# Kernel tuning notes

Hardware: AMD Instinct MI355X
Metric: run time of the kernel (lower is better)

The kernel has to match this reference:

```python
import jax, jax.numpy as jnp
import numpy as np

B = 131072   # batch (tokens)
D = 512      # d_model
P = 10       # n_programs
H = D // 4   # extractor hidden
MAXO = 4     # max operands
MAXR = 3     # max results


def setup_inputs() -> dict:
    key = jax.random.key(0)
    ks = jax.random.split(key, 6)
    hidden = jax.random.normal(ks[0], (B, D), jnp.float32)
    program_ids = jax.random.randint(ks[1], (B,), 0, P)
    Wr = jax.random.normal(ks[2], (D, P), jnp.float32) * (1.0 / np.sqrt(D))
    br = jnp.zeros((P,), jnp.float32)
    # stacked per-program extractor MLPs, output padded to MAXO (extra cols unused)
    W1 = jax.random.normal(ks[3], (P, D, H), jnp.float32) * (1.0 / np.sqrt(D))
    b1 = jnp.zeros((P, H), jnp.float32)
    W2 = jax.random.normal(ks[4], (P, H, MAXO), jnp.float32) * (1.0 / np.sqrt(H))
    b2 = jnp.zeros((P, MAXO), jnp.float32)
    return {"hidden": hidden, "program_ids": program_ids, "Wr": Wr, "br": br,
            "W1": W1, "b1": b1, "W2": W2, "b2": b2}


def _time_decompose(total_minutes):
    days = jnp.floor(total_minutes / 1440.0)
    rem = total_minutes - days * 1440.0
    hours = jnp.floor(rem / 60.0)
    minutes = rem - hours * 60.0
    return hours, minutes, days


def _safe(b):
    # avoid NaN/Inf from zero denominators in Mod/FloorDiv
    return jnp.where(b == 0, 1.0, b)


def _programs():
    # (fn -> tuple of result arrays, n_operands), order matches DEFAULT_PROGRAMS
    return [
        (lambda a, b: (a + b,), 2),                                   # IntAdd
        (lambda a, b: (a - b,), 2),                                   # IntSub
        (lambda a, b: (a * b,), 2),                                   # IntMul
        (lambda a, b: (jnp.mod(a, _safe(b)),), 2),                    # Mod
        (lambda a, b: (jnp.floor(a / _safe(b)),), 2),                 # FloorDiv
        (lambda h1, m1, h2, m2: _time_decompose(h1 * 60 + m1 + h2 * 60 + m2), 4),          # TimeAdd
        (lambda h1, m1, h2, m2: _time_decompose(h1 * 60 + m1 - (h2 * 60 + m2)), 4),        # TimeSub
        (lambda h1, m1, h2, m2: _time_decompose(jnp.abs(h1 * 60 + m1 - (h2 * 60 + m2))), 4),  # DurationBetween
        (lambda a, b: ((a > b).astype(jnp.float32),), 2),             # Greater
        (lambda a, b: ((a == b).astype(jnp.float32),), 2),            # Equal
    ]


def _compute_results(ops_rounded):
    # ops_rounded: [P, B, MAXO] -> results_all [P, B, MAXR]
    outs = []
    for idx, (fn, nop) in enumerate(_programs()):
        args = [ops_rounded[idx, :, i] for i in range(nop)]
        res = fn(*args)
        cols = list(res) + [jnp.zeros_like(res[0])] * (MAXR - len(res))
        outs.append(jnp.stack(cols, axis=-1))  # [B, MAXR]
    return jnp.stack(outs, axis=0)  # [P, B, MAXR]


def reference(hidden, program_ids, Wr, br, W1, b1, W2, b2):
    router_logits = hidden @ Wr + br                                  # [B, P]
    pre = jnp.einsum('bd,pdh->pbh', hidden, W1) + b1[:, None, :]      # [P, B, H]
    ops = jnp.einsum('pbh,pho->pbo', jax.nn.gelu(pre, approximate=False), W2) + b2[:, None, :]  # [P, B, MAXO]
    ops_rounded = jnp.round(ops)  # round_ste forward = round
    results_all = _compute_results(ops_rounded)                       # [P, B, MAXR]
    # combine: each row takes the result of its own program (masked scatter in torch)
    results = results_all[program_ids, jnp.arange(hidden.shape[0])]   # [B, MAXR]
    results = jax.lax.stop_gradient(results)  # torch .detach()
    return results, router_logits, ops, program_ids
```

## Files before the change

kernel.cpp:

```cpp
#include <hip/hip_runtime.h>
#include <math.h>

constexpr int D_   = 512;
constexpr int H_   = 128;
constexpr int P_   = 10;
constexpr int MAXO = 4;
constexpr int BM   = 128;
constexpr int BK   = 32;

typedef _Float16 f16;
typedef f16 f16x4 __attribute__((ext_vector_type(4)));
typedef f16 f16x8 __attribute__((ext_vector_type(8)));
typedef float f32x4 __attribute__((ext_vector_type(4)));

__device__ __forceinline__ float gelu_exact(float x) {
    return 0.5f * x * (1.0f + erff(x * 0.70710678118654752f));
}

__device__ __forceinline__ void time_decomp(float t, float& hr, float& mi, float& dy) {
    float days = floorf(t / 1440.0f);
    float rem  = t - days * 1440.0f;
    float hours = floorf(rem / 60.0f);
    float minutes = rem - hours * 60.0f;
    hr = hours; mi = minutes; dy = days;
}

__device__ __forceinline__ void g2l16(const f16* g, f16* l) {
    __builtin_amdgcn_global_load_lds(
        (const __attribute__((address_space(1))) void*)g,
        (__attribute__((address_space(3))) void*)l, 16, 0, 0);
}

__global__ __launch_bounds__(256) void cvt_w1_kernel(
    const float* __restrict__ W1, f16* __restrict__ hi, f16* __restrict__ lo)
{
    int i = blockIdx.x * 256 + threadIdx.x;
    float x = W1[i];
    f16 h = (f16)x;
    f16 L = (f16)(x - (float)h);
    int dh = i % (D_ * H_);
    int p  = i / (D_ * H_);
    int d  = dh / H_;
    int hh = dh % H_;
    size_t o = ((size_t)(p * H_ + hh)) * D_ + d;
    hi[o] = h; lo[o] = L;
}

template <bool WRITE_SPLIT>
__global__ __launch_bounds__(256) void router_cvt_kernel(
    const float* __restrict__ hidden, const float* __restrict__ Wr,
    const float* __restrict__ br, const int* __restrict__ pids,
    float* __restrict__ out_router, float* __restrict__ out_pids,
    f16* __restrict__ hidHi, f16* __restrict__ hidLo, int B)
{
    __shared__ float Wrs[D_ * 12];
    const int tid = threadIdx.x;
    for (int i = tid; i < D_ * P_; i += 256) {
        int k = i / P_;
        int q = i - k * P_;
        Wrs[k * 12 + q] = Wr[i];
    }
    __syncthreads();

    const int lane = tid & 63;
    const int wv   = tid >> 6;
    const int b    = blockIdx.x * 4 + wv;
    const float* hrow = hidden + (size_t)b * D_;

    float acc[P_];
#pragma unroll
    for (int q = 0; q < P_; ++q) acc[q] = 0.0f;

#pragma unroll
    for (int j = 0; j < 8; ++j) {
        int k = j * 64 + lane;
        float hv = hrow[k];
        if (WRITE_SPLIT) {
            f16 hh = (f16)hv;
            hidHi[(size_t)b * D_ + k] = hh;
            hidLo[(size_t)b * D_ + k] = (f16)(hv - (float)hh);
        }
        float wv12[12];
        *reinterpret_cast<float4*>(&wv12[0]) = *reinterpret_cast<const float4*>(&Wrs[k * 12 + 0]);
        *reinterpret_cast<float4*>(&wv12[4]) = *reinterpret_cast<const float4*>(&Wrs[k * 12 + 4]);
        *reinterpret_cast<float2*>(&wv12[8]) = *reinterpret_cast<const float2*>(&Wrs[k * 12 + 8]);
#pragma unroll
        for (int q = 0; q < P_; ++q) acc[q] = fmaf(hv, wv12[q], acc[q]);
    }

#pragma unroll
    for (int off = 1; off < 64; off <<= 1) {
#pragma unroll
        for (int q = 0; q < P_; ++q)
            acc[q] += __shfl_xor(acc[q], off, 64);
    }

    if (lane == 0) {
        float* o = out_router + (size_t)b * P_;
#pragma unroll
        for (int q = 0; q < P_; ++q) o[q] = acc[q] + br[q];
        out_pids[b] = (float)pids[b];
    }
}

template <bool PRECONV>
__global__ __launch_bounds__(512, 2) void extractor_kernel(
    const float* __restrict__ hidden,
    const f16*   __restrict__ hidHi,
    const f16*   __restrict__ hidLo,
    const int*   __restrict__ pids,
    const f16*   __restrict__ W1Thi,
    const f16*   __restrict__ W1Tlo,
    const float* __restrict__ b1,
    const float* __restrict__ W2,
    const float* __restrict__ b2,
    float* __restrict__ out_results,
    float* __restrict__ out_ops,
    int B)
{
    __shared__ __align__(16) char smem[71680];
    float* red = (float*)(smem + 65536);
    float* W2s = (float*)(smem + 69632);

    const int bid = blockIdx.x;
    const int ngroups = gridDim.x / P_;
    int g, p;
    if ((ngroups & 7) == 0) {
        const int gpx = ngroups >> 3;
        const int x   = bid & 7;
        const int q   = bid >> 3;
        g = x * gpx + q / P_;
        p = q % P_;
    } else {
        g = bid / P_;
        p = bid % P_;
    }
    const int b0  = g * BM;
    const int tid = threadIdx.x;
    const int l   = tid & 63;
    const int w   = tid >> 6;
    const int wm  = w >> 1, wn = w & 1;
    const int l15 = l & 15, l4 = l >> 4;

    const int sg8 = (((l & 3) ^ ((l >> 3) & 3))) * 8;
    const int rd8 = ((l4 ^ ((l15 >> 1) & 3))) * 8;

    if (tid < H_) {
        ((f32x4*)W2s)[tid] = ((const f32x4*)(W2 + (size_t)p * H_ * 4))[tid];
    }

    f32x4 acc[2][4];
#pragma unroll
    for (int mi = 0; mi < 2; ++mi)
#pragma unroll
        for (int ni = 0; ni < 4; ++ni) acc[mi][ni] = (f32x4){0.f, 0.f, 0.f, 0.f};

    const f16* Bhig = W1Thi + (size_t)p * H_ * D_;
    const f16* Blog = W1Tlo + (size_t)p * H_ * D_;

    auto stage = [&](int kc, char* buf) {
        f16* Ah = (f16*)(buf);
        f16* Al = (f16*)(buf + 8192);
        f16* Bh = (f16*)(buf + 16384);
        f16* Bl = (f16*)(buf + 24576);
        const int r0 = w * 16;
        size_t gb = (size_t)(r0 + (l >> 2)) * D_ + kc * BK + sg8;
        g2l16(Bhig + gb, Bh + r0 * BK);
        g2l16(Blog + gb, Bl + r0 * BK);
        if constexpr (PRECONV) {
            size_t ga = (size_t)(b0 + r0 + (l >> 2)) * D_ + kc * BK + sg8;
            g2l16(hidHi + ga, Ah + r0 * BK);
            g2l16(hidLo + ga, Al + r0 * BK);
        } else {
#pragma unroll
            for (int it = 0; it < 2; ++it) {
                int i  = tid + it * 512;
                int m  = i >> 3;
                int k4 = (i & 7) * 4;
                int ks = ((k4 >> 3) ^ ((m >> 1) & 3)) * 8 + (k4 & 7);
                f32x4 v = *(const f32x4*)(hidden + (size_t)(b0 + m) * D_ + kc * BK + k4);
                f16x4 vh, vl;
#pragma unroll
                for (int j = 0; j < 4; ++j) {
                    f16 hj = (f16)v[j];
                    vh[j] = hj;
                    vl[j] = (f16)(v[j] - (float)hj);
                }
                *(f16x4*)&Ah[m * BK + ks] = vh;
                *(f16x4*)&Al[m * BK + ks] = vl;
            }
        }
    };

    auto compute = [&](const char* buf) {
        const f16* Ah = (const f16*)(buf);
        const f16* Al = (const f16*)(buf + 8192);
        const f16* Bh = (const f16*)(buf + 16384);
        const f16* Bl = (const f16*)(buf + 24576);
        f16x8 bh[4], bl[4];
#pragma unroll
        for (int ni = 0; ni < 4; ++ni) {
            int hrow = wn * 64 + ni * 16 + l15;
            bh[ni] = *(const f16x8*)&Bh[hrow * BK + rd8];
            bl[ni] = *(const f16x8*)&Bl[hrow * BK + rd8];
        }
#pragma unroll
        for (int mi = 0; mi < 2; ++mi) {
            int mrow = wm * 32 + mi * 16 + l15;
            f16x8 a_h = *(const f16x8*)&Ah[mrow * BK + rd8];
            f16x8 a_l = *(const f16x8*)&Al[mrow * BK + rd8];
#pragma unroll
            for (int ni = 0; ni < 4; ++ni) {
                acc[mi][ni] = __builtin_amdgcn_mfma_f32_16x16x32_f16(a_l, bh[ni], acc[mi][ni], 0, 0, 0);
                acc[mi][ni] = __builtin_amdgcn_mfma_f32_16x16x32_f16(a_h, bl[ni], acc[mi][ni], 0, 0, 0);
                acc[mi][ni] = __builtin_amdgcn_mfma_f32_16x16x32_f16(a_h, bh[ni], acc[mi][ni], 0, 0, 0);
            }
        }
    };

    char* buf0 = smem;
    char* buf1 = smem + 32768;

    stage(0, buf0);
    asm volatile("s_waitcnt vmcnt(0)" ::: "memory");
    __builtin_amdgcn_s_barrier();
    for (int kc = 0; kc < 16; kc += 2) {
        stage(kc + 1, buf1);
        asm volatile("s_waitcnt vmcnt(4)" ::: "memory");
        __builtin_amdgcn_s_barrier();
        compute(buf0);
        __builtin_amdgcn_s_barrier();
        if (kc + 2 < 16) {
            stage(kc + 2, buf0);
            asm volatile("s_waitcnt vmcnt(4)" ::: "memory");
        } else {
            asm volatile("s_waitcnt vmcnt(0)" ::: "memory");
        }
        __builtin_amdgcn_s_barrier();
        compute(buf1);
        __builtin_amdgcn_s_barrier();
    }

    float b1v[4];
#pragma unroll
    for (int ni = 0; ni < 4; ++ni)
        b1v[ni] = b1[p * H_ + wn * 64 + ni * 16 + l15];

#pragma unroll
    for (int mi = 0; mi < 2; ++mi) {
        float po[4][4];
#pragma unroll
        for (int r = 0; r < 4; ++r)
#pragma unroll
            for (int o = 0; o < 4; ++o) po[r][o] = 0.0f;

#pragma unroll
        for (int ni = 0; ni < 4; ++ni) {
            int h = wn * 64 + ni * 16 + l15;
            f32x4 w4 = ((const f32x4*)W2s)[h];
#pragma unroll
            for (int r = 0; r < 4; ++r) {
                float gg = gelu_exact(acc[mi][ni][r] + b1v[ni]);
#pragma unroll
                for (int o = 0; o < 4; ++o) po[r][o] = fmaf(gg, w4[o], po[r][o]);
            }
        }
#pragma unroll
        for (int off = 1; off < 16; off <<= 1) {
#pragma unroll
            for (int r = 0; r < 4; ++r)
#pragma unroll
                for (int o = 0; o < 4; ++o)
                    po[r][o] += __shfl_xor(po[r][o], off, 64);
        }
        float v = po[0][0];
#pragma unroll
        for (int rr = 0; rr < 4; ++rr)
#pragma unroll
            for (int oo = 0; oo < 4; ++oo)
                if (l15 == rr * 4 + oo) v = po[rr][oo];
        red[(wn * 128 + wm * 32 + mi * 16 + l4 * 4 + (l15 >> 2)) * 4 + (l15 & 3)] = v;
    }
    __syncthreads();

    if (tid < BM) {
        int b = b0 + tid;
        const float* r0p = &red[(0 * 128 + tid) * 4];
        const float* r1p = &red[(1 * 128 + tid) * 4];
        float o0 = r0p[0] + r1p[0] + b2[p * 4 + 0];
        float o1 = r0p[1] + r1p[1] + b2[p * 4 + 1];
        float o2 = r0p[2] + r1p[2] + b2[p * 4 + 2];
        float o3 = r0p[3] + r1p[3] + b2[p * 4 + 3];
        *reinterpret_cast<float4*>(out_ops + ((size_t)p * B + b) * MAXO) =
            make_float4(o0, o1, o2, o3);

        if (pids[b] == p) {
            float a0 = rintf(o0), a1 = rintf(o1), a2 = rintf(o2), a3 = rintf(o3);
            float r0 = 0.0f, r1 = 0.0f, r2 = 0.0f;
            switch (p) {
                case 0: r0 = a0 + a1; break;
                case 1: r0 = a0 - a1; break;
                case 2: r0 = a0 * a1; break;
                case 3: {
                    float bs = (a1 == 0.0f) ? 1.0f : a1;
                    float m = fmodf(a0, bs);
                    if (m != 0.0f && ((m < 0.0f) != (bs < 0.0f))) m += bs;
                    r0 = m;
                } break;
                case 4: {
                    float bs = (a1 == 0.0f) ? 1.0f : a1;
                    r0 = floorf(a0 / bs);
                } break;
                case 5: { float tt = a0 * 60.0f + a1 + a2 * 60.0f + a3; time_decomp(tt, r0, r1, r2); } break;
                case 6: { float tt = a0 * 60.0f + a1 - (a2 * 60.0f + a3); time_decomp(tt, r0, r1, r2); } break;
                case 7: { float tt = fabsf(a0 * 60.0f + a1 - (a2 * 60.0f + a3)); time_decomp(tt, r0, r1, r2); } break;
                case 8: r0 = (a0 > a1) ? 1.0f : 0.0f; break;
                case 9: r0 = (a0 == a1) ? 1.0f : 0.0f; break;
            }
            size_t ob = (size_t)b * 3;
            out_results[ob + 0] = r0;
            out_results[ob + 1] = r1;
            out_results[ob + 2] = r2;
        }
    }
}

extern "C" void kernel_launch(void* const* d_in, const int* in_sizes, int n_in,
                              void* d_out, int out_size, void* d_ws, size_t ws_size,
                              hipStream_t stream) {
    const float* hidden = (const float*)d_in[0];
    const int*   pids   = (const int*)  d_in[1];
    const float* Wr     = (const float*)d_in[2];
    const float* br     = (const float*)d_in[3];
    const float* W1     = (const float*)d_in[4];
    const float* b1     = (const float*)d_in[5];
    const float* W2     = (const float*)d_in[6];
    const float* b2     = (const float*)d_in[7];

    const int B = in_sizes[1];

    float* out         = (float*)d_out;
    float* out_results = out;
    float* out_router  = out + (size_t)B * 3;
    float* out_ops     = out + (size_t)B * 13;
    float* out_pids    = out + (size_t)B * 13 + (size_t)P_ * B * MAXO;

    const size_t nW1  = (size_t)P_ * H_ * D_;
    const size_t nHid = (size_t)B * D_;
    const size_t need = (2 * nW1 + 2 * nHid) * sizeof(f16);

    f16* W1Thi = (f16*)d_ws;
    f16* W1Tlo = W1Thi + nW1;

    cvt_w1_kernel<<<(int)(nW1 / 256), 256, 0, stream>>>(W1, W1Thi, W1Tlo);

    if (ws_size >= need) {
        f16* hidHi = W1Tlo + nW1;
        f16* hidLo = hidHi + nHid;
        router_cvt_kernel<true><<<B / 4, 256, 0, stream>>>(
            hidden, Wr, br, pids, out_router, out_pids, hidHi, hidLo, B);
        extractor_kernel<true><<<(B / BM) * P_, 512, 0, stream>>>(
            hidden, hidHi, hidLo, pids, W1Thi, W1Tlo, b1, W2, b2,
            out_results, out_ops, B);
    } else {
        router_cvt_kernel<false><<<B / 4, 256, 0, stream>>>(
            hidden, Wr, br, pids, out_router, out_pids, nullptr, nullptr, B);
        extractor_kernel<false><<<(B / BM) * P_, 512, 0, stream>>>(
            hidden, nullptr, nullptr, pids, W1Thi, W1Tlo, b1, W2, b2,
            out_results, out_ops, B);
    }
}
```

Baseline: 758.4 us.

## Prepack fp16 low parts in MFMA fragment order and load them directly to registers

```diff
diff --git a/kernel.cpp b/kernel.cpp
--- a/kernel.cpp
+++ b/kernel.cpp
@@ -38,12 +38,14 @@
     float x = W1[i];
     f16 h = (f16)x;
     f16 L = (f16)(x - (float)h);
-    int dh = i % (D_ * H_);
-    int p  = i / (D_ * H_);
-    int d  = dh / H_;
-    int hh = dh % H_;
-    size_t o = ((size_t)(p * H_ + hh)) * D_ + d;
-    hi[o] = h; lo[o] = L;
+    int p   = i / (D_ * H_);
+    int rem = i % (D_ * H_);
+    int d   = rem / H_;
+    int hh  = rem % H_;
+    hi[((size_t)(p * H_ + hh)) * D_ + d] = h;
+    int kc = d >> 5, l4 = (d >> 3) & 3, j = d & 7;
+    int ni = hh >> 4, l15 = hh & 15;
+    lo[((((size_t)p * 16 + kc) * 8 + ni) * 64 + l4 * 16 + l15) * 8 + j] = L;
 }
 
 template <bool WRITE_SPLIT>
@@ -51,7 +53,7 @@
     const float* __restrict__ hidden, const float* __restrict__ Wr,
     const float* __restrict__ br, const int* __restrict__ pids,
     float* __restrict__ out_router, float* __restrict__ out_pids,
-    f16* __restrict__ hidHi, f16* __restrict__ hidLo, int B)
+    f16* __restrict__ hidHi, f16* __restrict__ hidLoP, int B)
 {
     __shared__ float Wrs[D_ * 12];
     const int tid = threadIdx.x;
@@ -66,6 +68,8 @@
     const int wv   = tid >> 6;
     const int b    = blockIdx.x * 4 + wv;
     const float* hrow = hidden + (size_t)b * D_;
+    const size_t tb  = (size_t)(b >> 4);
+    const int    l15b = b & 15;
 
     float acc[P_];
 #pragma unroll
@@ -78,7 +82,9 @@
         if (WRITE_SPLIT) {
             f16 hh = (f16)hv;
             hidHi[(size_t)b * D_ + k] = hh;
-            hidLo[(size_t)b * D_ + k] = (f16)(hv - (float)hh);
+            int kc = k >> 5, l4k = (k >> 3) & 3, jj = k & 7;
+            hidLoP[((tb * 16 + kc) * 64 + l4k * 16 + l15b) * 8 + jj] =
+                (f16)(hv - (float)hh);
         }
         float wv12[12];
         *reinterpret_cast<float4*>(&wv12[0]) = *reinterpret_cast<const float4*>(&Wrs[k * 12 + 0]);
@@ -107,10 +113,10 @@
 __global__ __launch_bounds__(512, 2) void extractor_kernel(
     const float* __restrict__ hidden,
     const f16*   __restrict__ hidHi,
-    const f16*   __restrict__ hidLo,
+    const f16*   __restrict__ hidLoP,
     const int*   __restrict__ pids,
     const f16*   __restrict__ W1Thi,
-    const f16*   __restrict__ W1Tlo,
+    const f16*   __restrict__ W1Slo,
     const float* __restrict__ b1,
     const float* __restrict__ W2,
     const float* __restrict__ b2,
@@ -118,9 +124,9 @@
     float* __restrict__ out_ops,
     int B)
 {
-    __shared__ __align__(16) char smem[71680];
-    float* red = (float*)(smem + 65536);
-    float* W2s = (float*)(smem + 69632);
+    __shared__ __align__(16) char smem[38912];
+    float* red = (float*)(smem + 32768);
+    float* W2s = (float*)(smem + 36864);
 
     const int bid = blockIdx.x;
     const int ngroups = gridDim.x / P_;
@@ -156,59 +162,57 @@
         for (int ni = 0; ni < 4; ++ni) acc[mi][ni] = (f32x4){0.f, 0.f, 0.f, 0.f};
 
     const f16* Bhig = W1Thi + (size_t)p * H_ * D_;
-    const f16* Blog = W1Tlo + (size_t)p * H_ * D_;
-
-    auto stage = [&](int kc, char* buf) {
+    const f16* BloBase = W1Slo + (((size_t)p * 16 * 8 + wn * 4) * 64 + l) * 8;
+    const int  tb0 = (b0 >> 4) + wm * 2;
+    const f16* AloBase = hidLoP + (((size_t)tb0 * 16) * 64 + l) * 8;
+
+    auto stageHi = [&](int kc, char* buf) {
         f16* Ah = (f16*)(buf);
-        f16* Al = (f16*)(buf + 8192);
-        f16* Bh = (f16*)(buf + 16384);
-        f16* Bl = (f16*)(buf + 24576);
+        f16* Bh = (f16*)(buf + 8192);
         const int r0 = w * 16;
         size_t gb = (size_t)(r0 + (l >> 2)) * D_ + kc * BK + sg8;
         g2l16(Bhig + gb, Bh + r0 * BK);
-        g2l16(Blog + gb, Bl + r0 * BK);
         if constexpr (PRECONV) {
             size_t ga = (size_t)(b0 + r0 + (l >> 2)) * D_ + kc * BK + sg8;
             g2l16(hidHi + ga, Ah + r0 * BK);
-            g2l16(hidLo + ga, Al + r0 * BK);
-        } else {
-#pragma unroll
-            for (int it = 0; it < 2; ++it) {
-                int i  = tid + it * 512;
-                int m  = i >> 3;
-                int k4 = (i & 7) * 4;
-                int ks = ((k4 >> 3) ^ ((m >> 1) & 3)) * 8 + (k4 & 7);
-                f32x4 v = *(const f32x4*)(hidden + (size_t)(b0 + m) * D_ + kc * BK + k4);
-                f16x4 vh, vl;
+        }
+    };
+    auto loadLo = [&](int kc, f16x8* bl, f16x8* al) {
+        const f16* bp = BloBase + (size_t)kc * 4096;
+#pragma unroll
+        for (int ni = 0; ni < 4; ++ni)
+            bl[ni] = *(const f16x8*)(bp + ni * 512);
+        if constexpr (PRECONV) {
+            const f16* ap = AloBase + (size_t)kc * 512;
+            al[0] = *(const f16x8*)(ap);
+            al[1] = *(const f16x8*)(ap + 8192);
+        }
+    };
+
+    auto compute = [&](const char* buf, const f16x8* bl, const f16x8* al, int kc) {
+        const f16* Ah = (const f16*)(buf);
+        const f16* Bh = (const f16*)(buf + 8192);
+        f16x8 bh[4];
+#pragma unroll
+        for (int ni = 0; ni < 4; ++ni)
+            bh[ni] = *(const f16x8*)&Bh[(wn * 64 + ni * 16 + l15) * BK + rd8];
+#pragma unroll
+        for (int mi = 0; mi < 2; ++mi) {
+            f16x8 a_h, a_l;
+            if constexpr (PRECONV) {
+                a_h = *(const f16x8*)&Ah[(wm * 32 + mi * 16 + l15) * BK + rd8];
+                a_l = al[mi];
+            } else {
+                const float* rp = hidden + (size_t)(b0 + wm * 32 + mi * 16 + l15) * D_
+                                 + kc * BK + l4 * 8;
+                f32x4 x0 = *(const f32x4*)rp;
+                f32x4 x1 = *(const f32x4*)(rp + 4);
 #pragma unroll
                 for (int j = 0; j < 4; ++j) {
-                    f16 hj = (f16)v[j];
-                    vh[j] = hj;
-                    vl[j] = (f16)(v[j] - (float)hj);
+                    f16 h0 = (f16)x0[j]; a_h[j] = h0; a_l[j] = (f16)(x0[j] - (float)h0);
+                    f16 h1 = (f16)x1[j]; a_h[j + 4] = h1; a_l[j + 4] = (f16)(x1[j] - (float)h1);
                 }
-                *(f16x4*)&Ah[m * BK + ks] = vh;
-                *(f16x4*)&Al[m * BK + ks] = vl;
             }
-        }
-    };
-
-    auto compute = [&](const char* buf) {
-        const f16* Ah = (const f16*)(buf);
-        const f16* Al = (const f16*)(buf + 8192);
-        const f16* Bh = (const f16*)(buf + 16384);
-        const f16* Bl = (const f16*)(buf + 24576);
-        f16x8 bh[4], bl[4];
-#pragma unroll
-        for (int ni = 0; ni < 4; ++ni) {
-            int hrow = wn * 64 + ni * 16 + l15;
-            bh[ni] = *(const f16x8*)&Bh[hrow * BK + rd8];
-            bl[ni] = *(const f16x8*)&Bl[hrow * BK + rd8];
-        }
-#pragma unroll
-        for (int mi = 0; mi < 2; ++mi) {
-            int mrow = wm * 32 + mi * 16 + l15;
-            f16x8 a_h = *(const f16x8*)&Ah[mrow * BK + rd8];
-            f16x8 a_l = *(const f16x8*)&Al[mrow * BK + rd8];
 #pragma unroll
             for (int ni = 0; ni < 4; ++ni) {
                 acc[mi][ni] = __builtin_amdgcn_mfma_f32_16x16x32_f16(a_l, bh[ni], acc[mi][ni], 0, 0, 0);
@@ -219,25 +223,31 @@
     };
 
     char* buf0 = smem;
-    char* buf1 = smem + 32768;
-
-    stage(0, buf0);
+    char* buf1 = smem + 16384;
+    f16x8 blA[4], alA[2], blB[4], alB[2];
+
+    stageHi(0, buf0);
+    loadLo(0, blA, alA);
     asm volatile("s_waitcnt vmcnt(0)" ::: "memory");
     __builtin_amdgcn_s_barrier();
     for (int kc = 0; kc < 16; kc += 2) {
-        stage(kc + 1, buf1);
-        asm volatile("s_waitcnt vmcnt(4)" ::: "memory");
+        stageHi(kc + 1, buf1);
+        loadLo(kc + 1, blB, alB);
+        if constexpr (PRECONV) asm volatile("s_waitcnt vmcnt(8)" ::: "memory");
+        else                   asm volatile("s_waitcnt vmcnt(5)" ::: "memory");
         __builtin_amdgcn_s_barrier();
-        compute(buf0);
+        compute(buf0, blA, alA, kc);
         __builtin_amdgcn_s_barrier();
         if (kc + 2 < 16) {
-            stage(kc + 2, buf0);
-            asm volatile("s_waitcnt vmcnt(4)" ::: "memory");
+            stageHi(kc + 2, buf0);
+            loadLo(kc + 2, blA, alA);
+            if constexpr (PRECONV) asm volatile("s_waitcnt vmcnt(8)" ::: "memory");
+            else                   asm volatile("s_waitcnt vmcnt(5)" ::: "memory");
         } else {
             asm volatile("s_waitcnt vmcnt(0)" ::: "memory");
         }
         __builtin_amdgcn_s_barrier();
-        compute(buf1);
+        compute(buf1, blB, alB, kc + 1);
         __builtin_amdgcn_s_barrier();
     }
 
@@ -350,23 +360,23 @@
     const size_t need = (2 * nW1 + 2 * nHid) * sizeof(f16);
 
     f16* W1Thi = (f16*)d_ws;
-    f16* W1Tlo = W1Thi + nW1;
-
-    cvt_w1_kernel<<<(int)(nW1 / 256), 256, 0, stream>>>(W1, W1Thi, W1Tlo);
+    f16* W1Slo = W1Thi + nW1;
+
+    cvt_w1_kernel<<<(int)(nW1 / 256), 256, 0, stream>>>(W1, W1Thi, W1Slo);
 
     if (ws_size >= need) {
-        f16* hidHi = W1Tlo + nW1;
-        f16* hidLo = hidHi + nHid;
+        f16* hidHi  = W1Slo + nW1;
+        f16* hidLoP = hidHi + nHid;
         router_cvt_kernel<true><<<B / 4, 256, 0, stream>>>(
-            hidden, Wr, br, pids, out_router, out_pids, hidHi, hidLo, B);
+            hidden, Wr, br, pids, out_router, out_pids, hidHi, hidLoP, B);
         extractor_kernel<true><<<(B / BM) * P_, 512, 0, stream>>>(
-            hidden, hidHi, hidLo, pids, W1Thi, W1Tlo, b1, W2, b2,
+            hidden, hidHi, hidLoP, pids, W1Thi, W1Slo, b1, W2, b2,
             out_results, out_ops, B);
     } else {
         router_cvt_kernel<false><<<B / 4, 256, 0, stream>>>(
             hidden, Wr, br, pids, out_router, out_pids, nullptr, nullptr, B);
         extractor_kernel<false><<<(B / BM) * P_, 512, 0, stream>>>(
-            hidden, nullptr, nullptr, pids, W1Thi, W1Tlo, b1, W2, b2,
+            hidden, nullptr, nullptr, pids, W1Thi, W1Slo, b1, W2, b2,
             out_results, out_ops, B);
     }
 }
```

After: 998.8 us. +31.7%, slower.

## Store hidden splits in MFMA fragment order and load A directly to registers

Applied to the files above, without the earlier changes.

```diff
diff --git a/kernel.cpp b/kernel.cpp
--- a/kernel.cpp
+++ b/kernel.cpp
@@ -51,7 +51,7 @@
     const float* __restrict__ hidden, const float* __restrict__ Wr,
     const float* __restrict__ br, const int* __restrict__ pids,
     float* __restrict__ out_router, float* __restrict__ out_pids,
-    f16* __restrict__ hidHi, f16* __restrict__ hidLo, int B)
+    f16* __restrict__ hidFhi, f16* __restrict__ hidFlo, int B)
 {
     __shared__ float Wrs[D_ * 12];
     const int tid = threadIdx.x;
@@ -66,6 +66,8 @@
     const int wv   = tid >> 6;
     const int b    = blockIdx.x * 4 + wv;
     const float* hrow = hidden + (size_t)b * D_;
+    const size_t t16  = (size_t)(b >> 4);
+    const int    r15  = b & 15;
 
     float acc[P_];
 #pragma unroll
@@ -76,9 +78,11 @@
         int k = j * 64 + lane;
         float hv = hrow[k];
         if (WRITE_SPLIT) {
+            int kc = k >> 5, l4k = (k >> 3) & 3, jj = k & 7;
+            size_t off = ((t16 * 16 + kc) * 64 + l4k * 16 + r15) * 8 + jj;
             f16 hh = (f16)hv;
-            hidHi[(size_t)b * D_ + k] = hh;
-            hidLo[(size_t)b * D_ + k] = (f16)(hv - (float)hh);
+            hidFhi[off] = hh;
+            hidFlo[off] = (f16)(hv - (float)hh);
         }
         float wv12[12];
         *reinterpret_cast<float4*>(&wv12[0]) = *reinterpret_cast<const float4*>(&Wrs[k * 12 + 0]);
@@ -106,8 +110,8 @@
 template <bool PRECONV>
 __global__ __launch_bounds__(512, 2) void extractor_kernel(
     const float* __restrict__ hidden,
-    const f16*   __restrict__ hidHi,
-    const f16*   __restrict__ hidLo,
+    const f16*   __restrict__ hidFhi,
+    const f16*   __restrict__ hidFlo,
     const int*   __restrict__ pids,
     const f16*   __restrict__ W1Thi,
     const f16*   __restrict__ W1Tlo,
@@ -118,9 +122,9 @@
     float* __restrict__ out_ops,
     int B)
 {
-    __shared__ __align__(16) char smem[71680];
-    float* red = (float*)(smem + 65536);
-    float* W2s = (float*)(smem + 69632);
+    __shared__ __align__(16) char smem[38912];
+    float* red = (float*)(smem + 32768);
+    float* W2s = (float*)(smem + 36864);
 
     const int bid = blockIdx.x;
     const int ngroups = gridDim.x / P_;
@@ -158,45 +162,30 @@
     const f16* Bhig = W1Thi + (size_t)p * H_ * D_;
     const f16* Blog = W1Tlo + (size_t)p * H_ * D_;
 
-    auto stage = [&](int kc, char* buf) {
-        f16* Ah = (f16*)(buf);
-        f16* Al = (f16*)(buf + 8192);
-        f16* Bh = (f16*)(buf + 16384);
-        f16* Bl = (f16*)(buf + 24576);
+    auto stageB = [&](int kc, char* buf) {
+        f16* Bh = (f16*)(buf);
+        f16* Bl = (f16*)(buf + 8192);
         const int r0 = w * 16;
         size_t gb = (size_t)(r0 + (l >> 2)) * D_ + kc * BK + sg8;
         g2l16(Bhig + gb, Bh + r0 * BK);
         g2l16(Blog + gb, Bl + r0 * BK);
+    };
+
+    auto loadA = [&](int kc, f16x8* aH, f16x8* aL) {
         if constexpr (PRECONV) {
-            size_t ga = (size_t)(b0 + r0 + (l >> 2)) * D_ + kc * BK + sg8;
-            g2l16(hidHi + ga, Ah + r0 * BK);
-            g2l16(hidLo + ga, Al + r0 * BK);
-        } else {
-#pragma unroll
-            for (int it = 0; it < 2; ++it) {
-                int i  = tid + it * 512;
-                int m  = i >> 3;
-                int k4 = (i & 7) * 4;
-                int ks = ((k4 >> 3) ^ ((m >> 1) & 3)) * 8 + (k4 & 7);
-                f32x4 v = *(const f32x4*)(hidden + (size_t)(b0 + m) * D_ + kc * BK + k4);
-                f16x4 vh, vl;
-#pragma unroll
-                for (int j = 0; j < 4; ++j) {
-                    f16 hj = (f16)v[j];
-                    vh[j] = hj;
-                    vl[j] = (f16)(v[j] - (float)hj);
-                }
-                *(f16x4*)&Ah[m * BK + ks] = vh;
-                *(f16x4*)&Al[m * BK + ks] = vl;
+#pragma unroll
+            for (int mi = 0; mi < 2; ++mi) {
+                const size_t off =
+                    (((size_t)(b0 / 16 + wm * 2 + mi) * 16 + kc) * 64 + l) * 8;
+                aH[mi] = *(const f16x8*)(hidFhi + off);
+                aL[mi] = *(const f16x8*)(hidFlo + off);
             }
         }
     };
 
-    auto compute = [&](const char* buf) {
-        const f16* Ah = (const f16*)(buf);
-        const f16* Al = (const f16*)(buf + 8192);
-        const f16* Bh = (const f16*)(buf + 16384);
-        const f16* Bl = (const f16*)(buf + 24576);
+    auto compute = [&](const char* buf, const f16x8* aH, const f16x8* aL, int kc) {
+        const f16* Bh = (const f16*)(buf);
+        const f16* Bl = (const f16*)(buf + 8192);
         f16x8 bh[4], bl[4];
 #pragma unroll
         for (int ni = 0; ni < 4; ++ni) {
@@ -206,9 +195,20 @@
         }
 #pragma unroll
         for (int mi = 0; mi < 2; ++mi) {
-            int mrow = wm * 32 + mi * 16 + l15;
-            f16x8 a_h = *(const f16x8*)&Ah[mrow * BK + rd8];
-            f16x8 a_l = *(const f16x8*)&Al[mrow * BK + rd8];
+            f16x8 a_h, a_l;
+            if constexpr (PRECONV) {
+                a_h = aH[mi]; a_l = aL[mi];
+            } else {
+                const float* rp = hidden + (size_t)(b0 + wm * 32 + mi * 16 + l15) * D_
+                                 + kc * BK + l4 * 8;
+                f32x4 x0 = *(const f32x4*)rp;
+                f32x4 x1 = *(const f32x4*)(rp + 4);
+#pragma unroll
+                for (int j = 0; j < 4; ++j) {
+                    f16 h0 = (f16)x0[j]; a_h[j] = h0; a_l[j] = (f16)(x0[j] - (float)h0);
+                    f16 h1 = (f16)x1[j]; a_h[j + 4] = h1; a_l[j + 4] = (f16)(x1[j] - (float)h1);
+                }
+            }
 #pragma unroll
             for (int ni = 0; ni < 4; ++ni) {
                 acc[mi][ni] = __builtin_amdgcn_mfma_f32_16x16x32_f16(a_l, bh[ni], acc[mi][ni], 0, 0, 0);
@@ -219,26 +219,42 @@
     };
 
     char* buf0 = smem;
-    char* buf1 = smem + 32768;
-
-    stage(0, buf0);
-    asm volatile("s_waitcnt vmcnt(0)" ::: "memory");
-    __builtin_amdgcn_s_barrier();
-    for (int kc = 0; kc < 16; kc += 2) {
-        stage(kc + 1, buf1);
-        asm volatile("s_waitcnt vmcnt(4)" ::: "memory");
+    char* buf1 = smem + 16384;
+    f16x8 aHa[2], aLa[2], aHb[2], aLb[2];
+
+    if constexpr (PRECONV) {
+        loadA(0, aHa, aLa);
+        stageB(0, buf0);
+        asm volatile("s_waitcnt vmcnt(0)" ::: "memory");
         __builtin_amdgcn_s_barrier();
-        compute(buf0);
-        __builtin_amdgcn_s_barrier();
-        if (kc + 2 < 16) {
-            stage(kc + 2, buf0);
-            asm volatile("s_waitcnt vmcnt(4)" ::: "memory");
-        } else {
-            asm volatile("s_waitcnt vmcnt(0)" ::: "memory");
-        }
-        __builtin_amdgcn_s_barrier();
-        compute(buf1);
-        __builtin_amdgcn_s_barrier();
+        for (int kc = 0; kc < 16; kc += 2) {
+            loadA(kc + 1, aHb, aLb);
+            stageB(kc + 1, buf1);
+            asm volatile("s_waitcnt vmcnt(6)" ::: "memory");
+            __builtin_amdgcn_s_barrier();
+            compute(buf0, aHa, aLa, kc);
+            __builtin_amdgcn_s_barrier();
+            if (kc + 2 < 16) {
+                loadA(kc + 2, aHa, aLa);
+                stageB(kc + 2, buf0);
+                asm volatile("s_waitcnt vmcnt(6)" ::: "memory");
+            } else {
+                asm volatile("s_waitcnt vmcnt(0)" ::: "memory");
+            }
+            __builtin_amdgcn_s_barrier();
+            compute(buf1, aHb, aLb, kc + 1);
+            __builtin_amdgcn_s_barrier();
+        }
+    } else {
+        stageB(0, buf0);
+        __syncthreads();
+        for (int kc = 0; kc < 16; ++kc) {
+            char* cur = (kc & 1) ? buf1 : buf0;
+            char* nxt = (kc & 1) ? buf0 : buf1;
+            if (kc < 15) stageB(kc + 1, nxt);
+            compute(cur, aHa, aLa, kc);
+            __syncthreads();
+        }
     }
 
     float b1v[4];
@@ -355,12 +371,12 @@
     cvt_w1_kernel<<<(int)(nW1 / 256), 256, 0, stream>>>(W1, W1Thi, W1Tlo);
 
     if (ws_size >= need) {
-        f16* hidHi = W1Tlo + nW1;
-        f16* hidLo = hidHi + nHid;
+        f16* hidFhi = W1Tlo + nW1;
+        f16* hidFlo = hidFhi + nHid;
         router_cvt_kernel<true><<<B / 4, 256, 0, stream>>>(
-            hidden, Wr, br, pids, out_router, out_pids, hidHi, hidLo, B);
+            hidden, Wr, br, pids, out_router, out_pids, hidFhi, hidFlo, B);
         extractor_kernel<true><<<(B / BM) * P_, 512, 0, stream>>>(
-            hidden, hidHi, hidLo, pids, W1Thi, W1Tlo, b1, W2, b2,
+            hidden, hidFhi, hidFlo, pids, W1Thi, W1Tlo, b1, W2, b2,
             out_results, out_ops, B);
     } else {
         router_cvt_kernel<false><<<B / 4, 256, 0, stream>>>(
```

Result: slower. 791.2 us (+4.3%).
